# Kernel tuning notes

Measured on AMD Instinct MI355X. Metric: run time of the kernel, lower is better.

Reference implementation:

```python
import jax, jax.numpy as jnp
import numpy as np
from jax import lax

# dims per init_kwargs / input_specs
V, D, N, W, B, T = 32000, 512, 250000, 64, 4, 1024
LOOPS, THRESH = 4, 0.99


def _ln(x, scale, bias):
    m = jnp.mean(x, -1, keepdims=True)
    v = jnp.var(x, -1, keepdims=True)
    return (x - m) * lax.rsqrt(v + 1e-5) * scale + bias


def setup_inputs() -> dict:
    key = jax.random.key(0)
    ks = jax.random.split(key, 12)
    s = 0.02
    p = lambda k, shape: jax.random.normal(k, shape, jnp.float32) * s
    return {
        "input_ids": jax.random.randint(ks[0], (B, T), 0, V),
        "embed": p(ks[1], (V, D)),
        "enc_w": p(ks[2], (D, D)), "enc_b": jnp.zeros((D,), jnp.float32),
        "ln_enc_s": jnp.ones((D,), jnp.float32), "ln_enc_b": jnp.zeros((D,), jnp.float32),
        "idx_w": p(ks[3], (D, D)), "idx_b": jnp.zeros((D,), jnp.float32),
        "mu_w": p(ks[4], (D, 1)), "mu_b": jnp.zeros((1,), jnp.float32),
        "sig_w": p(ks[5], (D, 1)), "sig_b": jnp.zeros((1,), jnp.float32),
        "pool_table": p(ks[6], (N, D)),
        "int_w1": p(ks[7], (2 * D, D)), "int_b1": jnp.zeros((D,), jnp.float32),
        "int_w2": p(ks[8], (D, D)), "int_b2": jnp.zeros((D,), jnp.float32),
        "ln_s": jnp.ones((D,), jnp.float32), "ln_b": jnp.zeros((D,), jnp.float32),
        "halt_w": p(ks[9], (D, 1)), "halt_b": jnp.zeros((1,), jnp.float32),
        "dec_w": p(ks[10], (D, V)), "dec_b": jnp.zeros((V,), jnp.float32),
    }


def reference(input_ids, embed, enc_w, enc_b, ln_enc_s, ln_enc_b,
              idx_w, idx_b, mu_w, mu_b, sig_w, sig_b, pool_table,
              int_w1, int_b1, int_w2, int_b2, ln_s, ln_b,
              halt_w, halt_b, dec_w, dec_b):
    # TinyController.encode: embed -> Dense -> gelu -> LayerNorm
    hidden = _ln(jax.nn.gelu(embed[input_ids] @ enc_w + enc_b), ln_enc_s, ln_enc_b)  # [B,T,D]
    state = hidden
    dt = hidden.dtype
    halt_prob = jnp.zeros((B, T, 1), dt)
    halted = jnp.zeros((B, T, 1), dt)
    idxs = []
    for _ in range(LOOPS):  # fixed small loop count, unrolled
        prev = state
        pooled = jnp.mean(state, axis=1)                       # [B,D]
        h = jax.nn.gelu(pooled @ idx_w + idx_b)
        mu = jax.nn.sigmoid(h @ mu_w + mu_b)                   # [B,1], coord in [0,1]
        sigma = jax.nn.softplus(h @ sig_w + sig_b) + 1e-4      # [B,1]
        # CoordinateMassivePool: contiguous window of W rows around mu*N
        center = mu[:, 0] * N
        start = jnp.clip(jnp.floor(center - W / 2).astype(jnp.int32), 0, N - W)  # [B]
        window = jax.vmap(lambda s: lax.dynamic_slice(pool_table, (s, 0), (W, D)))(start)  # [B,W,D]
        pos = (start[:, None] + jnp.arange(W)[None, :]).astype(dt) / N            # [B,W]
        w = jnp.exp(-0.5 * ((pos - mu) / sigma) ** 2)
        w = w / jnp.sum(w, axis=-1, keepdims=True)
        retrieved = jnp.einsum('bw,bwd->bd', w, window)        # [B,D]
        combined = jnp.concatenate(
            [state, jnp.broadcast_to(retrieved[:, None, :], (B, T, D))], axis=-1)  # [B,T,2D]
        integrated = _ln(jax.nn.gelu(combined @ int_w1 + int_b1) @ int_w2 + int_b2, ln_s, ln_b)
        candidate = state + integrated
        # ACT halting
        p_halt = jax.nn.sigmoid(candidate @ halt_w + halt_b)   # [B,T,1]
        halt_prob = halt_prob + p_halt * (1.0 - halted)
        new_halted = (halt_prob > THRESH).astype(dt)
        state = (1.0 - halted) * candidate + halted * prev
        halted = new_halted
        idxs.append(start)
    logits = state @ dec_w + dec_b                             # [B,T,V]
    all_indices = jnp.stack(idxs, axis=1)                      # [B,LOOPS]
    return logits, all_indices
```

## Files before the change

### kernel.cpp

```cpp
#include <hip/hip_runtime.h>

#define DEV __device__ __forceinline__

typedef __attribute__((ext_vector_type(8))) short bf16x8;
typedef __attribute__((ext_vector_type(4))) float f32x4;

typedef const __attribute__((address_space(1))) void* gsrc_t;
typedef __attribute__((address_space(3))) void* gdst_t;

DEV void gld16(const void* g, void* l){ __builtin_amdgcn_global_load_lds((gsrc_t)g,(gdst_t)l,16,0,0); }
DEV void gld4 (const void* g, void* l){ __builtin_amdgcn_global_load_lds((gsrc_t)g,(gdst_t)l, 4,0,0); }

DEV unsigned short f2bf(float f){
  union { float f; unsigned int u; } x; x.f = f;
  unsigned int u = x.u;
  return (unsigned short)((u + 0x7fffu + ((u >> 16) & 1u)) >> 16);
}
DEV unsigned long long pack4bf(float a, float b, float c, float d){
  return (unsigned long long)f2bf(a)
       | ((unsigned long long)f2bf(b) << 16)
       | ((unsigned long long)f2bf(c) << 32)
       | ((unsigned long long)f2bf(d) << 48);
}
DEV float gelu_t(float x){
  float u = 0.7978845608028654f * (x + 0.044715f * x * x * x);
  return 0.5f * x * (1.0f + tanhf(u));
}
DEV float sigmoidf_(float x){ return 1.0f / (1.0f + expf(-x)); }

DEV void BAR_TOP(){ __builtin_amdgcn_s_barrier(); asm volatile("" ::: "memory"); }
DEV void BAR_END(){
  __builtin_amdgcn_sched_barrier(0);
  asm volatile("s_waitcnt lgkmcnt(0)" ::: "memory");
  __builtin_amdgcn_s_barrier();
  asm volatile("" ::: "memory");
}

__global__ __launch_bounds__(256) void kPrep(const float* __restrict__ dec_w,
                                             unsigned short* __restrict__ dec_wT,
                                             const float* __restrict__ s0, const float* __restrict__ s1,
                                             const float* __restrict__ s2,
                                             unsigned short* __restrict__ d0, unsigned short* __restrict__ d1,
                                             unsigned short* __restrict__ d2,
                                             const int* __restrict__ ids,
                                             const float* __restrict__ embed,
                                             unsigned short* __restrict__ E){
  __shared__ float t[64][65];
  const int bid = blockIdx.x, tid = threadIdx.x;
  if (bid < 4000){
    int n0 = (bid % 500) * 64, k0 = (bid / 500) * 64;
    #pragma unroll
    for (int i = 0; i < 16; i++){
      int idx = i * 256 + tid; int r = idx >> 6, c = idx & 63;
      t[r][c] = dec_w[(size_t)(k0 + r) * 32000 + n0 + c];
    }
    __syncthreads();
    #pragma unroll
    for (int i = 0; i < 16; i++){
      int idx = i * 256 + tid; int r = idx >> 6, c = idx & 63;
      dec_wT[(size_t)(n0 + r) * 512 + k0 + c] = f2bf(t[c][r]);
    }
  } else if (bid < 4192){
    int rel = bid - 4000;
    int z = rel >> 6, rem = rel & 63;
    const float* W = (z == 0) ? s0 : (z == 1) ? s1 : s2;
    unsigned short* D = (z == 0) ? d0 : (z == 1) ? d1 : d2;
    int n0 = (rem & 7) * 64, k0 = (rem >> 3) * 64;
    #pragma unroll
    for (int i = 0; i < 16; i++){
      int idx = i * 256 + tid; int r = idx >> 6, c = idx & 63;
      t[r][c] = W[(size_t)(k0 + r) * 512 + n0 + c];
    }
    __syncthreads();
    #pragma unroll
    for (int i = 0; i < 16; i++){
      int idx = i * 256 + tid; int r = idx >> 6, c = idx & 63;
      D[(size_t)(n0 + r) * 512 + k0 + c] = f2bf(t[c][r]);
    }
  } else {
    int idx = bid - 4192;
    int row = idx * 2 + (tid >> 7);
    int t2  = tid & 127;
    int id = ids[row];
    float4 v = ((const float4*)(embed + (size_t)id * 512))[t2];
    *(unsigned long long*)(E + (size_t)row * 512 + t2 * 4) = pack4bf(v.x, v.y, v.z, v.w);
  }
}

template<int ENC>
__global__ __launch_bounds__(512) void kGemmLN(
    const unsigned short* __restrict__ A, const unsigned short* __restrict__ BT,
    const float* __restrict__ bias, const float* __restrict__ lns, const float* __restrict__ lnb,
    const float* __restrict__ hw, const float* __restrict__ hb,
    float* __restrict__ st, unsigned short* __restrict__ stb,
    float* __restrict__ part, float* __restrict__ halt_p, float* __restrict__ halted){
  __shared__ alignas(16) unsigned short lA[2][32 * 32];
  __shared__ alignas(16) unsigned short lB[2][512 * 32];
  __shared__ float pS[8][32], pQ[8][32], pH[8][32];
  __shared__ float sMean[32], sRs[32], sFac[32];
  const int tid = threadIdx.x, w = tid >> 6, lane = tid & 63;
  const int q = lane >> 4, c = lane & 15, lk8 = q * 8;
  const int r0 = blockIdx.x * 32;
  const int ar = tid >> 4, ak = (tid & 15) * 2;
  const int br = tid >> 2, bk = (tid & 3) * 8;
  f32x4 acc[2][4] = {};

  auto STAGE = [&](int buf, int k0){
    gld4 (A  + (size_t)(r0 + ar) * 512 + k0 + ak, &lA[buf][ar * 32 + ak]);
    #pragma unroll
    for (int i = 0; i < 4; i++)
      gld16(BT + (size_t)(i * 128 + br) * 512 + k0 + bk, &lB[buf][(i * 512 + tid) * 8]);
  };

  STAGE(0, 0);
  #pragma unroll
  for (int t = 0; t < 16; t++){
    if (t < 15){
      STAGE((t + 1) & 1, (t + 1) * 32);
      asm volatile("s_waitcnt vmcnt(5)" ::: "memory");
    } else {
      asm volatile("s_waitcnt vmcnt(0)" ::: "memory");
    }
    BAR_TOP();
    const unsigned short* la = lA[t & 1];
    const unsigned short* lb = lB[t & 1];
    bf16x8 af[2], bfv[4];
    #pragma unroll
    for (int m = 0; m < 2; m++) af[m]  = *(const bf16x8*)&la[(m * 16 + c) * 32 + lk8];
    #pragma unroll
    for (int n = 0; n < 4; n++) bfv[n] = *(const bf16x8*)&lb[(w * 64 + n * 16 + c) * 32 + lk8];
    #pragma unroll
    for (int m = 0; m < 2; m++)
      #pragma unroll
      for (int n = 0; n < 4; n++)
        acc[m][n] = __builtin_amdgcn_mfma_f32_16x16x32_bf16(af[m], bfv[n], acc[m][n], 0, 0, 0);
    BAR_END();
  }

  #pragma unroll
  for (int n = 0; n < 4; n++){
    float bcol = bias[w * 64 + n * 16 + c];
    #pragma unroll
    for (int m = 0; m < 2; m++)
      #pragma unroll
      for (int r = 0; r < 4; r++){
        float v = acc[m][n][r] + bcol;
        if (ENC) v = gelu_t(v);
        acc[m][n][r] = v;
      }
  }
  float rS[2][4], rQ[2][4];
  #pragma unroll
  for (int m = 0; m < 2; m++)
    #pragma unroll
    for (int r = 0; r < 4; r++){
      float s = 0.f, s2 = 0.f;
      #pragma unroll
      for (int n = 0; n < 4; n++){ float v = acc[m][n][r]; s += v; s2 += v * v; }
      rS[m][r] = s; rQ[m][r] = s2;
    }
  #pragma unroll
  for (int mask = 1; mask < 16; mask <<= 1)
    #pragma unroll
    for (int m = 0; m < 2; m++)
      #pragma unroll
      for (int r = 0; r < 4; r++){
        rS[m][r] += __shfl_xor(rS[m][r], mask);
        rQ[m][r] += __shfl_xor(rQ[m][r], mask);
      }
  if (c == 0)
    #pragma unroll
    for (int m = 0; m < 2; m++)
      #pragma unroll
      for (int r = 0; r < 4; r++){
        pS[w][m * 16 + q * 4 + r] = rS[m][r];
        pQ[w][m * 16 + q * 4 + r] = rQ[m][r];
      }
  __syncthreads();
  if (tid < 32){
    float s = 0.f, s2 = 0.f;
    #pragma unroll
    for (int v = 0; v < 8; v++){ s += pS[v][tid]; s2 += pQ[v][tid]; }
    float mean = s * (1.f / 512.f);
    float var  = s2 * (1.f / 512.f) - mean * mean;
    sMean[tid] = mean; sRs[tid] = rsqrtf(var + 1e-5f);
    if (ENC){ halt_p[r0 + tid] = 0.f; halted[r0 + tid] = 0.f; }
  }
  __syncthreads();
  float lnsv[4], lnbv[4];
  #pragma unroll
  for (int n = 0; n < 4; n++){ lnsv[n] = lns[w * 64 + n * 16 + c]; lnbv[n] = lnb[w * 64 + n * 16 + c]; }
  #pragma unroll
  for (int m = 0; m < 2; m++)
    #pragma unroll
    for (int r = 0; r < 4; r++){
      int row = m * 16 + q * 4 + r;
      float mu = sMean[row], rs = sRs[row];
      #pragma unroll
      for (int n = 0; n < 4; n++)
        acc[m][n][r] = (acc[m][n][r] - mu) * rs * lnsv[n] + lnbv[n];
    }

  float sold[2][4][4];
  if (!ENC){
    float hwv[4];
    #pragma unroll
    for (int n = 0; n < 4; n++) hwv[n] = hw[w * 64 + n * 16 + c];
    #pragma unroll
    for (int m = 0; m < 2; m++)
      #pragma unroll
      for (int r = 0; r < 4; r++){
        int row = m * 16 + q * 4 + r;
        #pragma unroll
        for (int n = 0; n < 4; n++)
          sold[m][n][r] = st[(size_t)(r0 + row) * 512 + w * 64 + n * 16 + c];
      }
    float rH[2][4];
    #pragma unroll
    for (int m = 0; m < 2; m++)
      #pragma unroll
      for (int r = 0; r < 4; r++){
        float d = 0.f;
        #pragma unroll
        for (int n = 0; n < 4; n++) d += (sold[m][n][r] + acc[m][n][r]) * hwv[n];
        rH[m][r] = d;
      }
    #pragma unroll
    for (int mask = 1; mask < 16; mask <<= 1)
      #pragma unroll
      for (int m = 0; m < 2; m++)
        #pragma unroll
        for (int r = 0; r < 4; r++) rH[m][r] += __shfl_xor(rH[m][r], mask);
    if (c == 0)
      #pragma unroll
      for (int m = 0; m < 2; m++)
        #pragma unroll
        for (int r = 0; r < 4; r++) pH[w][m * 16 + q * 4 + r] = rH[m][r];
    __syncthreads();
    if (tid < 32){
      float d = 0.f;
      #pragma unroll
      for (int v = 0; v < 8; v++) d += pH[v][tid];
      float hd = halted[r0 + tid];
      float p  = sigmoidf_(d + hb[0]);
      float hp = halt_p[r0 + tid] + p * (1.f - hd);
      halt_p[r0 + tid] = hp;
      halted[r0 + tid] = (hp > 0.99f) ? 1.f : 0.f;
      sFac[tid] = 1.f - hd;
    }
    __syncthreads();
    #pragma unroll
    for (int m = 0; m < 2; m++)
      #pragma unroll
      for (int r = 0; r < 4; r++){
        int row = m * 16 + q * 4 + r;
        float f = sFac[row];
        #pragma unroll
        for (int n = 0; n < 4; n++)
          acc[m][n][r] = sold[m][n][r] + f * acc[m][n][r];
      }
  }

  #pragma unroll
  for (int m = 0; m < 2; m++)
    #pragma unroll
    for (int r = 0; r < 4; r++){
      int row = r0 + m * 16 + q * 4 + r;
      #pragma unroll
      for (int n = 0; n < 4; n++){
        int col = w * 64 + n * 16 + c;
        float v = acc[m][n][r];
        st [(size_t)row * 512 + col] = v;
        stb[(size_t)row * 512 + col] = f2bf(v);
      }
    }
  #pragma unroll
  for (int n = 0; n < 4; n++){
    float s = 0.f;
    #pragma unroll
    for (int m = 0; m < 2; m++)
      #pragma unroll
      for (int r = 0; r < 4; r++) s += acc[m][n][r];
    s += __shfl_xor(s, 16);
    s += __shfl_xor(s, 32);
    if (q == 0) part[(size_t)blockIdx.x * 512 + w * 64 + n * 16 + c] = s;
  }
}

__global__ __launch_bounds__(256) void kGemm64(const unsigned short* __restrict__ A,
                                               const unsigned short* __restrict__ BT,
                                               const float* __restrict__ rb,
                                               unsigned short* __restrict__ C){
  __shared__ alignas(16) unsigned short lA[2][64 * 32];
  __shared__ alignas(16) unsigned short lB[2][64 * 32];
  const int tid = threadIdx.x, w = tid >> 6, lane = tid & 63;
  const int q = lane >> 4, c = lane & 15, lk8 = q * 8;
  const int wm = w >> 1, wn = w & 1;
  const int m0 = blockIdx.y * 64, n0 = blockIdx.x * 64;
  const int sr = tid >> 2, sk = (tid & 3) * 8;
  f32x4 acc[2][2] = {};

  auto STAGE = [&](int buf, int k0){
    gld16(A  + (size_t)(m0 + sr) * 512 + k0 + sk, &lA[buf][tid * 8]);
    gld16(BT + (size_t)(n0 + sr) * 512 + k0 + sk, &lB[buf][tid * 8]);
  };

  STAGE(0, 0);
  #pragma unroll
  for (int t = 0; t < 16; t++){
    if (t < 15){
      STAGE((t + 1) & 1, (t + 1) * 32);
      asm volatile("s_waitcnt vmcnt(2)" ::: "memory");
    } else {
      asm volatile("s_waitcnt vmcnt(0)" ::: "memory");
    }
    BAR_TOP();
    bf16x8 af[2], bfv[2];
    #pragma unroll
    for (int m = 0; m < 2; m++) af[m]  = *(const bf16x8*)&lA[t & 1][(wm * 32 + m * 16 + c) * 32 + lk8];
    #pragma unroll
    for (int n = 0; n < 2; n++) bfv[n] = *(const bf16x8*)&lB[t & 1][(wn * 32 + n * 16 + c) * 32 + lk8];
    #pragma unroll
    for (int m = 0; m < 2; m++)
      #pragma unroll
      for (int n = 0; n < 2; n++)
        acc[m][n] = __builtin_amdgcn_mfma_f32_16x16x32_bf16(af[m], bfv[n], acc[m][n], 0, 0, 0);
    BAR_END();
  }

  #pragma unroll
  for (int m = 0; m < 2; m++)
    #pragma unroll
    for (int n = 0; n < 2; n++)
      #pragma unroll
      for (int r = 0; r < 4; r++){
        int row = m0 + wm * 32 + m * 16 + q * 4 + r;
        int col = n0 + wn * 32 + n * 16 + c;
        float v = acc[m][n][r] + rb[((row >> 10) << 9) + col];
        C[(size_t)row * 512 + col] = f2bf(gelu_t(v));
      }
}

__global__ __launch_bounds__(256) void kGemmDec(const unsigned short* __restrict__ A,
                                                const unsigned short* __restrict__ BT,
                                                const float* __restrict__ bias,
                                                float* __restrict__ C){
  __shared__ alignas(16) unsigned short lA[2][2][128 * 32];
  __shared__ alignas(16) unsigned short lB[2][2][128 * 32];
  const int tid = threadIdx.x, w = tid >> 6, lane = tid & 63;
  const int wm = w >> 1, wn = w & 1;
  const int c = lane & 15, q = lane >> 4;
  const int rk8 = (q ^ ((c >> 1) & 3)) * 8;
  int flat = blockIdx.x;
  flat = (flat & 7) * 1000 + (flat >> 3);
  const int m0 = (flat & 31) * 128;
  const int n0 = (flat >> 5) * 128;
  const int srow  = tid >> 2;
  const int skoff = ((tid & 3) ^ ((srow >> 1) & 3)) * 8;
  const int sdst  = srow * 32 + (tid & 3) * 8;
  f32x4 acc[4][4] = {};

  auto STG = [&](const unsigned short* M, unsigned short* dst, int base, int k0s){
    gld16(M + (size_t)(base + srow) * 512 + k0s + skoff, dst + sdst);
    gld16(M + (size_t)(base + 64 + srow) * 512 + k0s + skoff, dst + 64 * 32 + sdst);
  };

  STG(A,  &lA[0][0][0], m0, 0);
  STG(BT, &lB[0][0][0], n0, 0);
  STG(A,  &lA[0][1][0], m0, 32);
  STG(BT, &lB[0][1][0], n0, 32);

  for (int t = 0; t < 8; t++){
    const int buf = t & 1, nbuf = buf ^ 1;
    const int nk0 = (t + 1) * 64;
    #pragma unroll
    for (int s = 0; s < 2; s++){
      if (t == 7 && s == 1) asm volatile("s_waitcnt vmcnt(0)" ::: "memory");
      else                  asm volatile("s_waitcnt vmcnt(4)" ::: "memory");
      __builtin_amdgcn_s_barrier();
      asm volatile("" ::: "memory");
      bf16x8 af[4], bfr[4];
      #pragma unroll
      for (int mf = 0; mf < 4; mf++)
        af[mf] = *(const bf16x8*)&lA[buf][s][(wm * 64 + mf * 16 + c) * 32 + rk8];
      #pragma unroll
      for (int nf = 0; nf < 4; nf++)
        bfr[nf] = *(const bf16x8*)&lB[buf][s][(wn * 64 + nf * 16 + c) * 32 + rk8];
      if (t < 7){
        STG(A,  &lA[nbuf][s][0], m0, nk0 + s * 32);
        STG(BT, &lB[nbuf][s][0], n0, nk0 + s * 32);
      }
      asm volatile("s_waitcnt lgkmcnt(0)" ::: "memory");
      __builtin_amdgcn_sched_barrier(0);
      __builtin_amdgcn_s_setprio(1);
      #pragma unroll
      for (int mf = 0; mf < 4; mf++)
        #pragma unroll
        for (int nf = 0; nf < 4; nf++)
          acc[mf][nf] = __builtin_amdgcn_mfma_f32_16x16x32_bf16(af[mf], bfr[nf], acc[mf][nf], 0, 0, 0);
      __builtin_amdgcn_s_setprio(0);
    }
  }

  #pragma unroll
  for (int mf = 0; mf < 4; mf++){
    int rbase = m0 + wm * 64 + mf * 16 + q * 4;
    #pragma unroll
    for (int nf = 0; nf < 4; nf++){
      int col = n0 + wn * 64 + nf * 16 + c;
      float bcol = bias[col];
      #pragma unroll
      for (int r = 0; r < 4; r++)
        __builtin_nontemporal_store(acc[mf][nf][r] + bcol,
                                    &C[(size_t)(rbase + r) * 32000 + col]);
    }
  }
}

__global__ __launch_bounds__(512) void kCtl(const float* __restrict__ part,
                                            const float* __restrict__ idx_w, const float* __restrict__ idx_b,
                                            const float* __restrict__ mu_w, const float* __restrict__ mu_b,
                                            const float* __restrict__ sig_w, const float* __restrict__ sig_b,
                                            const float* __restrict__ pool_table,
                                            const float* __restrict__ w1b, const float* __restrict__ int_b1,
                                            float* __restrict__ r2, float* __restrict__ outIdx, int loop){
  __shared__ float xs[512];
  __shared__ float red[512];
  __shared__ float red2[512];
  __shared__ float evals[64];
  __shared__ float sc[4];
  int b = blockIdx.x, tid = threadIdx.x;

  float s = 0.f;
  #pragma unroll 8
  for (int c2 = 0; c2 < 32; c2++) s += part[(size_t)(b * 32 + c2) * 512 + tid];
  xs[tid] = s * (1.0f / 1024.0f);
  __syncthreads();

  float a = idx_b[tid];
  #pragma unroll 16
  for (int i = 0; i < 512; i++)
    a = fmaf(xs[i], idx_w[(size_t)i * 512 + tid], a);
  float hv = gelu_t(a);
  red[tid]  = hv * mu_w[tid];
  red2[tid] = hv * sig_w[tid];
  __syncthreads();
  for (int off2 = 256; off2 > 0; off2 >>= 1){
    if (tid < off2){ red[tid] += red[tid + off2]; red2[tid] += red2[tid + off2]; }
    __syncthreads();
  }
  if (tid == 0){
    float mu = sigmoidf_(red[0] + mu_b[0]);
    float sg = log1pf(expf(red2[0] + sig_b[0])) + 1e-4f;
    float center = mu * 250000.0f;
    int stt = (int)floorf(center - 32.0f);
    stt = stt < 0 ? 0 : (stt > 250000 - 64 ? 250000 - 64 : stt);
    sc[0] = mu; sc[1] = sg; sc[2] = (float)stt;
    outIdx[b * 4 + loop] = (float)stt;
  }
  __syncthreads();
  if (tid < 64){
    float pos = (sc[2] + (float)tid) * (1.0f / 250000.0f);
    float z = (pos - sc[0]) / sc[1];
    evals[tid] = expf(-0.5f * z * z);
  }
  __syncthreads();
  if (tid == 0){
    float wsum = 0.f;
    for (int j = 0; j < 64; j++) wsum += evals[j];
    sc[3] = wsum;
  }
  __syncthreads();
  int stt = (int)sc[2];
  float r = 0.f;
  #pragma unroll 8
  for (int j = 0; j < 64; j++)
    r = fmaf(evals[j], pool_table[(size_t)(stt + j) * 512 + tid], r);
  r /= sc[3];
  __syncthreads();
  xs[tid] = r;
  __syncthreads();
  float a2 = int_b1[tid];
  #pragma unroll 16
  for (int i = 0; i < 512; i++)
    a2 = fmaf(xs[i], w1b[(size_t)i * 512 + tid], a2);
  r2[(size_t)b * 512 + tid] = a2;
}

extern "C" void kernel_launch(void* const* d_in, const int* in_sizes, int n_in,
                              void* d_out, int out_size, void* d_ws, size_t ws_size,
                              hipStream_t stream){
  (void)in_sizes; (void)n_in; (void)out_size; (void)ws_size;
  const int*   ids    = (const int*)  d_in[0];
  const float* embed  = (const float*)d_in[1];
  const float* enc_w  = (const float*)d_in[2];
  const float* enc_b  = (const float*)d_in[3];
  const float* ln_es  = (const float*)d_in[4];
  const float* ln_eb  = (const float*)d_in[5];
  const float* idx_w  = (const float*)d_in[6];
  const float* idx_b  = (const float*)d_in[7];
  const float* mu_w   = (const float*)d_in[8];
  const float* mu_b   = (const float*)d_in[9];
  const float* sig_w  = (const float*)d_in[10];
  const float* sig_b  = (const float*)d_in[11];
  const float* pool_t = (const float*)d_in[12];
  const float* int_w1 = (const float*)d_in[13];
  const float* int_b1 = (const float*)d_in[14];
  const float* int_w2 = (const float*)d_in[15];
  const float* int_b2 = (const float*)d_in[16];
  const float* ln_s   = (const float*)d_in[17];
  const float* ln_b   = (const float*)d_in[18];
  const float* halt_w = (const float*)d_in[19];
  const float* halt_b = (const float*)d_in[20];
  const float* dec_w  = (const float*)d_in[21];
  const float* dec_b  = (const float*)d_in[22];

  char* ws = (char*)d_ws;
  size_t off = 0;
  auto alloc = [&](size_t bytes)->char*{
    char* p = ws + off; off += (bytes + 255) & ~(size_t)255; return p;
  };
  unsigned short* dec_wT  = (unsigned short*)alloc(32000ull * 512 * 2);
  unsigned short* enc_wT  = (unsigned short*)alloc(512ull * 512 * 2);
  unsigned short* w1T     = (unsigned short*)alloc(512ull * 512 * 2);
  unsigned short* w2T     = (unsigned short*)alloc(512ull * 512 * 2);
  unsigned short* bufB    = (unsigned short*)alloc(4096ull * 512 * 2);
  float*          state   = (float*)alloc(4096ull * 512 * 4);
  unsigned short* state_b = (unsigned short*)alloc(4096ull * 512 * 2);
  float*          part    = (float*)alloc(128ull * 512 * 4);
  float*          r2      = (float*)alloc(4ull * 512 * 4);
  float*          halt_p  = (float*)alloc(4096 * 4);
  float*          halted  = (float*)alloc(4096 * 4);
  float*          outF    = (float*)d_out;

  hipLaunchKernelGGL(kPrep, dim3(6240), dim3(256), 0, stream,
                     dec_w, dec_wT, enc_w, int_w1, int_w2, enc_wT, w1T, w2T,
                     ids, embed, bufB);

  hipLaunchKernelGGL((kGemmLN<1>), dim3(128), dim3(512), 0, stream,
                     bufB, enc_wT, enc_b, ln_es, ln_eb,
                     (const float*)nullptr, (const float*)nullptr,
                     state, state_b, part, halt_p, halted);

  for (int l = 0; l < 4; l++){
    hipLaunchKernelGGL(kCtl, dim3(4), dim3(512), 0, stream, part, idx_w, idx_b,
                       mu_w, mu_b, sig_w, sig_b, pool_t,
                       int_w1 + 512 * 512, int_b1,
                       r2, outF + 131072000, l);
    hipLaunchKernelGGL(kGemm64, dim3(8, 64), dim3(256), 0, stream,
                       state_b, w1T, r2, bufB);
    hipLaunchKernelGGL((kGemmLN<0>), dim3(128), dim3(512), 0, stream,
                       bufB, w2T, int_b2, ln_s, ln_b, halt_w, halt_b,
                       state, state_b, part, halt_p, halted);
  }

  hipLaunchKernelGGL(kGemmDec, dim3(8000), dim3(256), 0, stream,
                     state_b, dec_wT, dec_b, (float*)d_out);
}
```

Measured before the change: 528.0 us.

## Halve GemmLN row tile to 16 rows and triple-buffer decoder GEMM pipeline

The fused GEMM+LayerNorm kernel now handles 16 rows per block instead of 32 and launches 256 blocks, which fills more of the compute units on a wide GPU. The partial-sum buffer and the controller reduction grow to 64 chunks per batch to match. Separately, the decoder GEMM changes from a double buffer with two sub-stages to a three-buffer ring with one 32-wide K step, prefetching two steps ahead. The trade-off is more redundant loads of the 512-wide B operand per row in GemmLN, and more barriers per K in the decoder GEMM.

```diff
diff --git a/kernel.cpp b/kernel.cpp
--- a/kernel.cpp
+++ b/kernel.cpp
@@ -9,7 +9,6 @@
 typedef __attribute__((address_space(3))) void* gdst_t;
 
 DEV void gld16(const void* g, void* l){ __builtin_amdgcn_global_load_lds((gsrc_t)g,(gdst_t)l,16,0,0); }
-DEV void gld4 (const void* g, void* l){ __builtin_amdgcn_global_load_lds((gsrc_t)g,(gdst_t)l, 4,0,0); }
 
 DEV unsigned short f2bf(float f){
   union { float f; unsigned int u; } x; x.f = f;
@@ -94,19 +93,19 @@
     const float* __restrict__ hw, const float* __restrict__ hb,
     float* __restrict__ st, unsigned short* __restrict__ stb,
     float* __restrict__ part, float* __restrict__ halt_p, float* __restrict__ halted){
-  __shared__ alignas(16) unsigned short lA[2][32 * 32];
+  __shared__ alignas(16) unsigned short lA[2][16 * 32];
   __shared__ alignas(16) unsigned short lB[2][512 * 32];
-  __shared__ float pS[8][32], pQ[8][32], pH[8][32];
-  __shared__ float sMean[32], sRs[32], sFac[32];
+  __shared__ float pS[8][16], pQ[8][16], pH[8][16];
+  __shared__ float sMean[16], sRs[16], sFac[16];
   const int tid = threadIdx.x, w = tid >> 6, lane = tid & 63;
   const int q = lane >> 4, c = lane & 15, lk8 = q * 8;
-  const int r0 = blockIdx.x * 32;
-  const int ar = tid >> 4, ak = (tid & 15) * 2;
+  const int r0 = blockIdx.x * 16;
   const int br = tid >> 2, bk = (tid & 3) * 8;
-  f32x4 acc[2][4] = {};
+  f32x4 acc[4] = {};
 
   auto STAGE = [&](int buf, int k0){
-    gld4 (A  + (size_t)(r0 + ar) * 512 + k0 + ak, &lA[buf][ar * 32 + ak]);
+    if (w == 0)
+      gld16(A + (size_t)(r0 + (lane >> 2)) * 512 + k0 + (lane & 3) * 8, &lA[buf][lane * 8]);
     #pragma unroll
     for (int i = 0; i < 4; i++)
       gld16(BT + (size_t)(i * 128 + br) * 512 + k0 + bk, &lB[buf][(i * 512 + tid) * 8]);
@@ -117,23 +116,20 @@
   for (int t = 0; t < 16; t++){
     if (t < 15){
       STAGE((t + 1) & 1, (t + 1) * 32);
-      asm volatile("s_waitcnt vmcnt(5)" ::: "memory");
+      if (w == 0) asm volatile("s_waitcnt vmcnt(5)" ::: "memory");
+      else        asm volatile("s_waitcnt vmcnt(4)" ::: "memory");
     } else {
       asm volatile("s_waitcnt vmcnt(0)" ::: "memory");
     }
     BAR_TOP();
-    const unsigned short* la = lA[t & 1];
-    const unsigned short* lb = lB[t & 1];
-    bf16x8 af[2], bfv[4];
-    #pragma unroll
-    for (int m = 0; m < 2; m++) af[m]  = *(const bf16x8*)&la[(m * 16 + c) * 32 + lk8];
-    #pragma unroll
-    for (int n = 0; n < 4; n++) bfv[n] = *(const bf16x8*)&lb[(w * 64 + n * 16 + c) * 32 + lk8];
-    #pragma unroll
-    for (int m = 0; m < 2; m++)
-      #pragma unroll
-      for (int n = 0; n < 4; n++)
-        acc[m][n] = __builtin_amdgcn_mfma_f32_16x16x32_bf16(af[m], bfv[n], acc[m][n], 0, 0, 0);
+    bf16x8 af = *(const bf16x8*)&lA[t & 1][c * 32 + lk8];
+    bf16x8 bfv[4];
+    #pragma unroll
+    for (int n = 0; n < 4; n++)
+      bfv[n] = *(const bf16x8*)&lB[t & 1][(w * 64 + n * 16 + c) * 32 + lk8];
+    #pragma unroll
+    for (int n = 0; n < 4; n++)
+      acc[n] = __builtin_amdgcn_mfma_f32_16x16x32_bf16(af, bfv[n], acc[n], 0, 0, 0);
     BAR_END();
   }
 
@@ -141,43 +137,32 @@
   for (int n = 0; n < 4; n++){
     float bcol = bias[w * 64 + n * 16 + c];
     #pragma unroll
-    for (int m = 0; m < 2; m++)
-      #pragma unroll
-      for (int r = 0; r < 4; r++){
-        float v = acc[m][n][r] + bcol;
-        if (ENC) v = gelu_t(v);
-        acc[m][n][r] = v;
-      }
-  }
-  float rS[2][4], rQ[2][4];
-  #pragma unroll
-  for (int m = 0; m < 2; m++)
-    #pragma unroll
     for (int r = 0; r < 4; r++){
-      float s = 0.f, s2 = 0.f;
-      #pragma unroll
-      for (int n = 0; n < 4; n++){ float v = acc[m][n][r]; s += v; s2 += v * v; }
-      rS[m][r] = s; rQ[m][r] = s2;
-    }
+      float v = acc[n][r] + bcol;
+      if (ENC) v = gelu_t(v);
+      acc[n][r] = v;
+    }
+  }
+  float rS[4], rQ[4];
+  #pragma unroll
+  for (int r = 0; r < 4; r++){
+    float s = 0.f, s2 = 0.f;
+    #pragma unroll
+    for (int n = 0; n < 4; n++){ float v = acc[n][r]; s += v; s2 += v * v; }
+    rS[r] = s; rQ[r] = s2;
+  }
   #pragma unroll
   for (int mask = 1; mask < 16; mask <<= 1)
     #pragma unroll
-    for (int m = 0; m < 2; m++)
-      #pragma unroll
-      for (int r = 0; r < 4; r++){
-        rS[m][r] += __shfl_xor(rS[m][r], mask);
-        rQ[m][r] += __shfl_xor(rQ[m][r], mask);
-      }
+    for (int r = 0; r < 4; r++){
+      rS[r] += __shfl_xor(rS[r], mask);
+      rQ[r] += __shfl_xor(rQ[r], mask);
+    }
   if (c == 0)
     #pragma unroll
-    for (int m = 0; m < 2; m++)
-      #pragma unroll
-      for (int r = 0; r < 4; r++){
-        pS[w][m * 16 + q * 4 + r] = rS[m][r];
-        pQ[w][m * 16 + q * 4 + r] = rQ[m][r];
-      }
-  __syncthreads();
-  if (tid < 32){
+    for (int r = 0; r < 4; r++){ pS[w][q * 4 + r] = rS[r]; pQ[w][q * 4 + r] = rQ[r]; }
+  __syncthreads();
+  if (tid < 16){
     float s = 0.f, s2 = 0.f;
     #pragma unroll
     for (int v = 0; v < 8; v++){ s += pS[v][tid]; s2 += pQ[v][tid]; }
@@ -191,53 +176,43 @@
   #pragma unroll
   for (int n = 0; n < 4; n++){ lnsv[n] = lns[w * 64 + n * 16 + c]; lnbv[n] = lnb[w * 64 + n * 16 + c]; }
   #pragma unroll
-  for (int m = 0; m < 2; m++)
-    #pragma unroll
-    for (int r = 0; r < 4; r++){
-      int row = m * 16 + q * 4 + r;
-      float mu = sMean[row], rs = sRs[row];
-      #pragma unroll
-      for (int n = 0; n < 4; n++)
-        acc[m][n][r] = (acc[m][n][r] - mu) * rs * lnsv[n] + lnbv[n];
-    }
-
-  float sold[2][4][4];
+  for (int r = 0; r < 4; r++){
+    int row = q * 4 + r;
+    float mu = sMean[row], rs = sRs[row];
+    #pragma unroll
+    for (int n = 0; n < 4; n++)
+      acc[n][r] = (acc[n][r] - mu) * rs * lnsv[n] + lnbv[n];
+  }
+
+  float sold[4][4];
   if (!ENC){
     float hwv[4];
     #pragma unroll
     for (int n = 0; n < 4; n++) hwv[n] = hw[w * 64 + n * 16 + c];
     #pragma unroll
-    for (int m = 0; m < 2; m++)
-      #pragma unroll
-      for (int r = 0; r < 4; r++){
-        int row = m * 16 + q * 4 + r;
-        #pragma unroll
-        for (int n = 0; n < 4; n++)
-          sold[m][n][r] = st[(size_t)(r0 + row) * 512 + w * 64 + n * 16 + c];
-      }
-    float rH[2][4];
-    #pragma unroll
-    for (int m = 0; m < 2; m++)
-      #pragma unroll
-      for (int r = 0; r < 4; r++){
-        float d = 0.f;
-        #pragma unroll
-        for (int n = 0; n < 4; n++) d += (sold[m][n][r] + acc[m][n][r]) * hwv[n];
-        rH[m][r] = d;
-      }
+    for (int r = 0; r < 4; r++){
+      int row = q * 4 + r;
+      #pragma unroll
+      for (int n = 0; n < 4; n++)
+        sold[n][r] = st[(size_t)(r0 + row) * 512 + w * 64 + n * 16 + c];
+    }
+    float rH[4];
+    #pragma unroll
+    for (int r = 0; r < 4; r++){
+      float d = 0.f;
+      #pragma unroll
+      for (int n = 0; n < 4; n++) d += (sold[n][r] + acc[n][r]) * hwv[n];
+      rH[r] = d;
+    }
     #pragma unroll
     for (int mask = 1; mask < 16; mask <<= 1)
       #pragma unroll
-      for (int m = 0; m < 2; m++)
-        #pragma unroll
-        for (int r = 0; r < 4; r++) rH[m][r] += __shfl_xor(rH[m][r], mask);
+      for (int r = 0; r < 4; r++) rH[r] += __shfl_xor(rH[r], mask);
     if (c == 0)
       #pragma unroll
-      for (int m = 0; m < 2; m++)
-        #pragma unroll
-        for (int r = 0; r < 4; r++) pH[w][m * 16 + q * 4 + r] = rH[m][r];
+      for (int r = 0; r < 4; r++) pH[w][q * 4 + r] = rH[r];
     __syncthreads();
-    if (tid < 32){
+    if (tid < 16){
       float d = 0.f;
       #pragma unroll
       for (int v = 0; v < 8; v++) d += pH[v][tid];
@@ -250,37 +225,30 @@
     }
     __syncthreads();
     #pragma unroll
-    for (int m = 0; m < 2; m++)
-      #pragma unroll
-      for (int r = 0; r < 4; r++){
-        int row = m * 16 + q * 4 + r;
-        float f = sFac[row];
-        #pragma unroll
-        for (int n = 0; n < 4; n++)
-          acc[m][n][r] = sold[m][n][r] + f * acc[m][n][r];
-      }
-  }
-
-  #pragma unroll
-  for (int m = 0; m < 2; m++)
-    #pragma unroll
     for (int r = 0; r < 4; r++){
-      int row = r0 + m * 16 + q * 4 + r;
-      #pragma unroll
-      for (int n = 0; n < 4; n++){
-        int col = w * 64 + n * 16 + c;
-        float v = acc[m][n][r];
-        st [(size_t)row * 512 + col] = v;
-        stb[(size_t)row * 512 + col] = f2bf(v);
-      }
-    }
+      float f = sFac[q * 4 + r];
+      #pragma unroll
+      for (int n = 0; n < 4; n++)
+        acc[n][r] = sold[n][r] + f * acc[n][r];
+    }
+  }
+
+  #pragma unroll
+  for (int r = 0; r < 4; r++){
+    int row = r0 + q * 4 + r;
+    #pragma unroll
+    for (int n = 0; n < 4; n++){
+      int col = w * 64 + n * 16 + c;
+      float v = acc[n][r];
+      st [(size_t)row * 512 + col] = v;
+      stb[(size_t)row * 512 + col] = f2bf(v);
+    }
+  }
   #pragma unroll
   for (int n = 0; n < 4; n++){
     float s = 0.f;
     #pragma unroll
-    for (int m = 0; m < 2; m++)
-      #pragma unroll
-      for (int r = 0; r < 4; r++) s += acc[m][n][r];
+    for (int r = 0; r < 4; r++) s += acc[n][r];
     s += __shfl_xor(s, 16);
     s += __shfl_xor(s, 32);
     if (q == 0) part[(size_t)blockIdx.x * 512 + w * 64 + n * 16 + c] = s;
@@ -345,8 +313,8 @@
                                                 const unsigned short* __restrict__ BT,
                                                 const float* __restrict__ bias,
                                                 float* __restrict__ C){
-  __shared__ alignas(16) unsigned short lA[2][2][128 * 32];
-  __shared__ alignas(16) unsigned short lB[2][2][128 * 32];
+  __shared__ alignas(16) unsigned short lA[3][128 * 32];
+  __shared__ alignas(16) unsigned short lB[3][128 * 32];
   const int tid = threadIdx.x, w = tid >> 6, lane = tid & 63;
   const int wm = w >> 1, wn = w & 1;
   const int c = lane & 15, q = lane >> 4;
@@ -360,46 +328,38 @@
   const int sdst  = srow * 32 + (tid & 3) * 8;
   f32x4 acc[4][4] = {};
 
-  auto STG = [&](const unsigned short* M, unsigned short* dst, int base, int k0s){
-    gld16(M + (size_t)(base + srow) * 512 + k0s + skoff, dst + sdst);
-    gld16(M + (size_t)(base + 64 + srow) * 512 + k0s + skoff, dst + 64 * 32 + sdst);
+  auto STAGE = [&](int buf, int k0){
+    gld16(A  + (size_t)(m0 + srow) * 512 + k0 + skoff,      &lA[buf][sdst]);
+    gld16(A  + (size_t)(m0 + 64 + srow) * 512 + k0 + skoff, &lA[buf][64 * 32 + sdst]);
+    gld16(BT + (size_t)(n0 + srow) * 512 + k0 + skoff,      &lB[buf][sdst]);
+    gld16(BT + (size_t)(n0 + 64 + srow) * 512 + k0 + skoff, &lB[buf][64 * 32 + sdst]);
   };
 
-  STG(A,  &lA[0][0][0], m0, 0);
-  STG(BT, &lB[0][0][0], n0, 0);
-  STG(A,  &lA[0][1][0], m0, 32);
-  STG(BT, &lB[0][1][0], n0, 32);
-
-  for (int t = 0; t < 8; t++){
-    const int buf = t & 1, nbuf = buf ^ 1;
-    const int nk0 = (t + 1) * 64;
-    #pragma unroll
-    for (int s = 0; s < 2; s++){
-      if (t == 7 && s == 1) asm volatile("s_waitcnt vmcnt(0)" ::: "memory");
-      else                  asm volatile("s_waitcnt vmcnt(4)" ::: "memory");
-      __builtin_amdgcn_s_barrier();
-      asm volatile("" ::: "memory");
-      bf16x8 af[4], bfr[4];
-      #pragma unroll
-      for (int mf = 0; mf < 4; mf++)
-        af[mf] = *(const bf16x8*)&lA[buf][s][(wm * 64 + mf * 16 + c) * 32 + rk8];
+  STAGE(0, 0);
+  STAGE(1, 32);
+  for (int t = 0; t < 16; t++){
+    const int buf = t % 3;
+    if (t < 15) asm volatile("s_waitcnt vmcnt(4)" ::: "memory");
+    else        asm volatile("s_waitcnt vmcnt(0)" ::: "memory");
+    __builtin_amdgcn_s_barrier();
+    asm volatile("" ::: "memory");
+    bf16x8 af[4], bfr[4];
+    #pragma unroll
+    for (int mf = 0; mf < 4; mf++)
+      af[mf] = *(const bf16x8*)&lA[buf][(wm * 64 + mf * 16 + c) * 32 + rk8];
+    #pragma unroll
+    for (int nf = 0; nf < 4; nf++)
+      bfr[nf] = *(const bf16x8*)&lB[buf][(wn * 64 + nf * 16 + c) * 32 + rk8];
+    if (t < 14) STAGE((t + 2) % 3, (t + 2) * 32);
+    asm volatile("s_waitcnt lgkmcnt(0)" ::: "memory");
+    __builtin_amdgcn_sched_barrier(0);
+    __builtin_amdgcn_s_setprio(1);
+    #pragma unroll
+    for (int mf = 0; mf < 4; mf++)
       #pragma unroll
       for (int nf = 0; nf < 4; nf++)
-        bfr[nf] = *(const bf16x8*)&lB[buf][s][(wn * 64 + nf * 16 + c) * 32 + rk8];
-      if (t < 7){
-        STG(A,  &lA[nbuf][s][0], m0, nk0 + s * 32);
-        STG(BT, &lB[nbuf][s][0], n0, nk0 + s * 32);
-      }
-      asm volatile("s_waitcnt lgkmcnt(0)" ::: "memory");
-      __builtin_amdgcn_sched_barrier(0);
-      __builtin_amdgcn_s_setprio(1);
-      #pragma unroll
-      for (int mf = 0; mf < 4; mf++)
-        #pragma unroll
-        for (int nf = 0; nf < 4; nf++)
-          acc[mf][nf] = __builtin_amdgcn_mfma_f32_16x16x32_bf16(af[mf], bfr[nf], acc[mf][nf], 0, 0, 0);
-      __builtin_amdgcn_s_setprio(0);
-    }
+        acc[mf][nf] = __builtin_amdgcn_mfma_f32_16x16x32_bf16(af[mf], bfr[nf], acc[mf][nf], 0, 0, 0);
+    __builtin_amdgcn_s_setprio(0);
   }
 
   #pragma unroll
@@ -433,7 +393,7 @@
 
   float s = 0.f;
   #pragma unroll 8
-  for (int c2 = 0; c2 < 32; c2++) s += part[(size_t)(b * 32 + c2) * 512 + tid];
+  for (int c2 = 0; c2 < 64; c2++) s += part[(size_t)(b * 64 + c2) * 512 + tid];
   xs[tid] = s * (1.0f / 1024.0f);
   __syncthreads();
 
@@ -527,7 +487,7 @@
   unsigned short* bufB    = (unsigned short*)alloc(4096ull * 512 * 2);
   float*          state   = (float*)alloc(4096ull * 512 * 4);
   unsigned short* state_b = (unsigned short*)alloc(4096ull * 512 * 2);
-  float*          part    = (float*)alloc(128ull * 512 * 4);
+  float*          part    = (float*)alloc(256ull * 512 * 4);
   float*          r2      = (float*)alloc(4ull * 512 * 4);
   float*          halt_p  = (float*)alloc(4096 * 4);
   float*          halted  = (float*)alloc(4096 * 4);
@@ -537,7 +497,7 @@
                      dec_w, dec_wT, enc_w, int_w1, int_w2, enc_wT, w1T, w2T,
                      ids, embed, bufB);
 
-  hipLaunchKernelGGL((kGemmLN<1>), dim3(128), dim3(512), 0, stream,
+  hipLaunchKernelGGL((kGemmLN<1>), dim3(256), dim3(512), 0, stream,
                      bufB, enc_wT, enc_b, ln_es, ln_eb,
                      (const float*)nullptr, (const float*)nullptr,
                      state, state_b, part, halt_p, halted);
@@ -549,7 +509,7 @@
                        r2, outF + 131072000, l);
     hipLaunchKernelGGL(kGemm64, dim3(8, 64), dim3(256), 0, stream,
                        state_b, w1T, r2, bufB);
-    hipLaunchKernelGGL((kGemmLN<0>), dim3(128), dim3(512), 0, stream,
+    hipLaunchKernelGGL((kGemmLN<0>), dim3(256), dim3(512), 0, stream,
                        bufB, w2T, int_b2, ln_s, ln_b, halt_w, halt_b,
                        state, state_b, part, halt_p, halted);
   }
```

After: 507.7 us. -3.8%, faster.
